# Performance work log

Hardware: AMD Instinct MI355X
Metric: run time of the kernel (lower is better)

## Reference

```python
import jax, jax.numpy as jnp
import numpy as np

B, S, D = 8, 4096, 1024


def setup_inputs() -> dict:
    key = jax.random.key(0)
    k = jax.random.split(key, 6)
    scale = 1.0 / np.sqrt(D)  # torch nn.Linear default init range
    x = jax.random.normal(k[0], (B, S, D), dtype=jnp.float32)
    mask = jnp.ones((B, S), dtype=jnp.float32)
    Wu = jax.random.uniform(k[1], (D, D), jnp.float32, -scale, scale)
    bu = jax.random.uniform(k[2], (D,), jnp.float32, -scale, scale)
    Wf = jax.random.uniform(k[3], (D, D), jnp.float32, -scale, scale)
    bf = jax.random.uniform(k[4], (D,), jnp.float32, -scale, scale)
    decay_param = jnp.zeros((1,), dtype=jnp.float32)
    return {"x": x, "mask": mask, "Wu": Wu, "bu": bu, "Wf": Wf, "bf": bf, "decay_param": decay_param}


def reference(x, mask, Wu, bu, Wf, bf, decay_param):
    # decay is a learned scalar in (0,1)
    decay = jax.nn.sigmoid(decay_param)[0]
    # Batch linear_update over all timesteps at once: (B,S,D)
    upd = jnp.einsum('bsd,ed->bse', x, Wu) + bu
    m = mask[..., None]  # (B,S,1)
    # mask-gated recurrence: mem_t = a_t * mem_{t-1} + b_t
    #   a_t = mask*decay + (1-mask),  b_t = mask*update
    a = m * decay + (1.0 - m)
    b = m * upd
    a_s = jnp.swapaxes(a, 0, 1)  # (S,B,1)
    b_s = jnp.swapaxes(b, 0, 1)  # (S,B,D)

    def step(mem, ab):
        a_t, b_t = ab
        mem = a_t * mem + b_t
        return mem, mem

    mem0 = jnp.zeros((B, D), dtype=x.dtype)
    _, mem_seq = jax.lax.scan(step, mem0, (a_s, b_s))  # (S,B,D)
    mem_seq = jnp.swapaxes(mem_seq, 0, 1)  # (B,S,D)
    # Batch linear_f over all timesteps
    out = jnp.einsum('bsd,ed->bse', mem_seq, Wf) + bf
    return out
```

## Files before the change

kernel.cpp:

```cpp
#include <hip/hip_runtime.h>
#include <hip/hip_bf16.h>
#include <math.h>

#define PB 8
#define PS 4096
#define PD 1024

typedef __attribute__((ext_vector_type(8))) short bf16x8;
typedef __attribute__((ext_vector_type(4))) float f32x4;

__device__ __forceinline__ ushort f2b(float f) {
    unsigned u = __float_as_uint(f);
    unsigned r = (u + 0x7FFFu + ((u >> 16) & 1u)) >> 16;
    return (ushort)r;
}
__device__ __forceinline__ float b2f(ushort h) {
    return __uint_as_float(((unsigned)h) << 16);
}

__device__ __forceinline__ void gl2lds16(const void* g, void* l) {
    __builtin_amdgcn_global_load_lds(
        (const __attribute__((address_space(1))) void*)g,
        (__attribute__((address_space(3))) void*)l, 16, 0, 0);
}

__global__ __launch_bounds__(256) void cvt_f32_bf16(const float* __restrict__ in,
                                                    ushort* __restrict__ out, int n) {
    int i = (blockIdx.x * 256 + threadIdx.x) * 4;
    if (i + 3 < n) {
        float4 v = *(const float4*)(in + i);
        ushort4 o;
        o.x = f2b(v.x); o.y = f2b(v.y); o.z = f2b(v.z); o.w = f2b(v.w);
        *(ushort4*)(out + i) = o;
    }
}

template <bool OUT_BF16>
__global__ __launch_bounds__(256) void gemm_bt(const ushort* __restrict__ A,
                                               const ushort* __restrict__ Bm,
                                               const float* __restrict__ bias,
                                               void* __restrict__ C,
                                               int M, int N, int K) {
    __shared__ ushort As[128 * 32];
    __shared__ ushort Bs[128 * 32];

    const int tid = threadIdx.x;
    const int lane = tid & 63;
    const int wave = tid >> 6;
    const int nbn = N >> 7;
    const int bn = blockIdx.x % nbn;
    const int bm = blockIdx.x / nbn;
    const int wm = wave >> 1, wn = wave & 1;
    const int l15 = lane & 15, quad = lane >> 4;

    const int e0 = wave * 512 + lane * 8;
    const int sr = e0 >> 5;
    const int sc = e0 & 31;
    const ushort* Ag = A + (size_t)(bm * 128 + sr) * K + sc;
    const ushort* Bg = Bm + (size_t)(bn * 128 + sr) * K + sc;
    ushort* Asw = As + wave * 512;
    ushort* Bsw = Bs + wave * 512;

    f32x4 acc[4][4];
#pragma unroll
    for (int i = 0; i < 4; ++i)
#pragma unroll
        for (int j = 0; j < 4; ++j) acc[i][j] = (f32x4){0.f, 0.f, 0.f, 0.f};

    for (int k0 = 0; k0 < K; k0 += 32) {
        __syncthreads();
        gl2lds16(Ag + k0, Asw);
        gl2lds16(Ag + k0 + (size_t)64 * K, Asw + 2048);
        gl2lds16(Bg + k0, Bsw);
        gl2lds16(Bg + k0 + (size_t)64 * K, Bsw + 2048);
        __syncthreads();

        bf16x8 af[4], bfr[4];
#pragma unroll
        for (int i = 0; i < 4; ++i)
            af[i] = *(const bf16x8*)(As + (wm * 64 + i * 16 + l15) * 32 + quad * 8);
#pragma unroll
        for (int j = 0; j < 4; ++j)
            bfr[j] = *(const bf16x8*)(Bs + (wn * 64 + j * 16 + l15) * 32 + quad * 8);
#pragma unroll
        for (int i = 0; i < 4; ++i)
#pragma unroll
            for (int j = 0; j < 4; ++j)
                acc[i][j] = __builtin_amdgcn_mfma_f32_16x16x32_bf16(af[i], bfr[j], acc[i][j], 0, 0, 0);
    }

    const int gm0 = bm * 128 + wm * 64;
    const int gn0 = bn * 128 + wn * 64;
    float bv[4];
#pragma unroll
    for (int j = 0; j < 4; ++j) bv[j] = bias[gn0 + j * 16 + l15];
#pragma unroll
    for (int i = 0; i < 4; ++i) {
#pragma unroll
        for (int j = 0; j < 4; ++j) {
            const int col = gn0 + j * 16 + l15;
#pragma unroll
            for (int r = 0; r < 4; ++r) {
                const int row = gm0 + i * 16 + quad * 4 + r;
                float v = acc[i][j][r] + bv[j];
                if (OUT_BF16)
                    ((ushort*)C)[(size_t)row * N + col] = f2b(v);
                else
                    ((float*)C)[(size_t)row * N + col] = v;
            }
        }
    }
}

__global__ __launch_bounds__(256) void scan_partial(const ushort* __restrict__ upd,
                                                    const float* __restrict__ mask,
                                                    const float* __restrict__ dp,
                                                    float* __restrict__ Bc,
                                                    float* __restrict__ Ac,
                                                    int S, int D, int C) {
    const int c = blockIdx.x % C;
    const int b = blockIdx.x / C;
    const int L = S / C;
    const int d0 = threadIdx.x * 4;
    const float decay = 1.f / (1.f + expf(-dp[0]));
    const ushort* up = upd + ((size_t)b * S + (size_t)c * L) * D + d0;
    const float* mp = mask + (size_t)b * S + (size_t)c * L;
    float aA = 1.f;
    float b0 = 0.f, b1 = 0.f, b2 = 0.f, b3 = 0.f;
    for (int s = 0; s < L; ++s) {
        float m = mp[s];
        float a = m * decay + (1.f - m);
        ushort4 u = *(const ushort4*)(up + (size_t)s * D);
        aA *= a;
        b0 = a * b0 + m * b2f(u.x);
        b1 = a * b1 + m * b2f(u.y);
        b2 = a * b2 + m * b2f(u.z);
        b3 = a * b3 + m * b2f(u.w);
    }
    *(float4*)(Bc + (size_t)blockIdx.x * D + d0) = make_float4(b0, b1, b2, b3);
    if (threadIdx.x == 0) Ac[blockIdx.x] = aA;
}

__global__ __launch_bounds__(256) void scan_prefix(const float* __restrict__ Ac,
                                                   const float* __restrict__ Bc,
                                                   float* __restrict__ Mn, int D, int C) {
    int gid = blockIdx.x * 256 + threadIdx.x;
    int b = gid / D;
    int d = gid - b * D;
    float mem = 0.f;
    for (int c = 0; c < C; ++c) {
        size_t idx = ((size_t)(b * C + c)) * D + d;
        Mn[idx] = mem;
        mem = Ac[b * C + c] * mem + Bc[idx];
    }
}

__global__ __launch_bounds__(256) void scan_final(const ushort* __restrict__ upd,
                                                  const float* __restrict__ mask,
                                                  const float* __restrict__ dp,
                                                  const float* __restrict__ Mn,
                                                  ushort* __restrict__ ms,
                                                  int S, int D, int C) {
    const int c = blockIdx.x % C;
    const int b = blockIdx.x / C;
    const int L = S / C;
    const int d0 = threadIdx.x * 4;
    const float decay = 1.f / (1.f + expf(-dp[0]));
    const ushort* up = upd + ((size_t)b * S + (size_t)c * L) * D + d0;
    ushort* op = ms + ((size_t)b * S + (size_t)c * L) * D + d0;
    const float* mp = mask + (size_t)b * S + (size_t)c * L;
    float4 m0 = *(const float4*)(Mn + (size_t)blockIdx.x * D + d0);
    float v0 = m0.x, v1 = m0.y, v2 = m0.z, v3 = m0.w;
    for (int s = 0; s < L; ++s) {
        float m = mp[s];
        float a = m * decay + (1.f - m);
        ushort4 u = *(const ushort4*)(up + (size_t)s * D);
        v0 = a * v0 + m * b2f(u.x);
        v1 = a * v1 + m * b2f(u.y);
        v2 = a * v2 + m * b2f(u.z);
        v3 = a * v3 + m * b2f(u.w);
        ushort4 o;
        o.x = f2b(v0); o.y = f2b(v1); o.z = f2b(v2); o.w = f2b(v3);
        *(ushort4*)(op + (size_t)s * D) = o;
    }
}

extern "C" void kernel_launch(void* const* d_in, const int* in_sizes, int n_in,
                              void* d_out, int out_size, void* d_ws, size_t ws_size,
                              hipStream_t stream) {
    const float* x    = (const float*)d_in[0];
    const float* mask = (const float*)d_in[1];
    const float* Wu   = (const float*)d_in[2];
    const float* bu   = (const float*)d_in[3];
    const float* Wf   = (const float*)d_in[4];
    const float* bfv  = (const float*)d_in[5];
    const float* dp   = (const float*)d_in[6];

    const int B = PB, S = PS, D = PD;
    const int M = B * S;
    const int C = 128;

    char* ws = (char*)d_ws;
    ushort* xb   = (ushort*)(ws);
    ushort* updb = (ushort*)(ws + 67108864);
    ushort* memb = (ushort*)(ws + 134217728);
    ushort* Wub  = (ushort*)(ws + 201326592);
    ushort* Wfb  = (ushort*)(ws + 203423744);
    float*  Bc   = (float*)(ws + 205520896);
    float*  Mn   = (float*)(ws + 209715200);
    float*  Ac   = (float*)(ws + 213909504);

    const int nx = B * S * D;
    cvt_f32_bf16<<<nx / 1024, 256, 0, stream>>>(x, xb, nx);
    cvt_f32_bf16<<<(D * D) / 1024, 256, 0, stream>>>(Wu, Wub, D * D);
    cvt_f32_bf16<<<(D * D) / 1024, 256, 0, stream>>>(Wf, Wfb, D * D);

    dim3 g1((M / 128) * (D / 128));
    gemm_bt<true><<<g1, 256, 0, stream>>>(xb, Wub, bu, (void*)updb, M, D, D);

    scan_partial<<<B * C, 256, 0, stream>>>(updb, mask, dp, Bc, Ac, S, D, C);
    scan_prefix<<<(B * D) / 256, 256, 0, stream>>>(Ac, Bc, Mn, D, C);
    scan_final<<<B * C, 256, 0, stream>>>(updb, mask, dp, Mn, memb, S, D, C);

    gemm_bt<false><<<g1, 256, 0, stream>>>(memb, Wfb, bfv, d_out, M, D, D);
}
```

Before: 509.5 us.

## Swizzle GEMM LDS layout, remap blocks per XCD, merge weight casts, halve scan chunks

The GEMM now XOR-swizzles the 16-byte column groups when loading global data into LDS and applies the matching swizzle when reading fragments, to cut LDS bank conflicts. Blocks are remapped so each of the 8 XCDs handles a contiguous range of M tiles, which should improve L2 reuse of the A rows. The two weight conversion kernels are merged into one launch. The scan chunk count drops from 128 to 64, giving fewer, longer chunks per batch, which changes the balance between parallelism and prefix-pass work.

Result: faster. 482.0 us (-5.4%).

```diff
diff --git a/kernel.cpp b/kernel.cpp
--- a/kernel.cpp
+++ b/kernel.cpp
@@ -35,6 +35,20 @@
     }
 }
 
+__global__ __launch_bounds__(256) void cvt_w2(const float* __restrict__ Wu,
+                                              const float* __restrict__ Wf,
+                                              ushort* __restrict__ Wub,
+                                              ushort* __restrict__ Wfb, int n) {
+    int i = (blockIdx.x * 256 + threadIdx.x) * 4;
+    const float* in = (i < n) ? Wu : Wf;
+    ushort* out = (i < n) ? Wub : Wfb;
+    int j = (i < n) ? i : i - n;
+    float4 v = *(const float4*)(in + j);
+    ushort4 o;
+    o.x = f2b(v.x); o.y = f2b(v.y); o.z = f2b(v.z); o.w = f2b(v.w);
+    *(ushort4*)(out + j) = o;
+}
+
 template <bool OUT_BF16>
 __global__ __launch_bounds__(256) void gemm_bt(const ushort* __restrict__ A,
                                                const ushort* __restrict__ Bm,
@@ -48,16 +62,17 @@
     const int lane = tid & 63;
     const int wave = tid >> 6;
     const int nbn = N >> 7;
-    const int bn = blockIdx.x % nbn;
-    const int bm = blockIdx.x / nbn;
+    const int xcd = blockIdx.x & 7;
+    const int g = blockIdx.x >> 3;
+    const int bm = xcd * ((M >> 7) >> 3) + g / nbn;
+    const int bn = g % nbn;
     const int wm = wave >> 1, wn = wave & 1;
     const int l15 = lane & 15, quad = lane >> 4;
 
-    const int e0 = wave * 512 + lane * 8;
-    const int sr = e0 >> 5;
-    const int sc = e0 & 31;
-    const ushort* Ag = A + (size_t)(bm * 128 + sr) * K + sc;
-    const ushort* Bg = Bm + (size_t)(bn * 128 + sr) * K + sc;
+    const int grow = wave * 16 + (lane >> 2);
+    const int gx = (lane & 3) ^ ((lane >> 3) & 3);
+    const ushort* Ag = A + (size_t)(bm * 128 + grow) * K + gx * 8;
+    const ushort* Bg = Bm + (size_t)(bn * 128 + grow) * K + gx * 8;
     ushort* Asw = As + wave * 512;
     ushort* Bsw = Bs + wave * 512;
 
@@ -66,6 +81,9 @@
     for (int i = 0; i < 4; ++i)
 #pragma unroll
         for (int j = 0; j < 4; ++j) acc[i][j] = (f32x4){0.f, 0.f, 0.f, 0.f};
+
+    const int rsw = (l15 >> 1) & 3;
+    const int aoff = (quad ^ rsw) * 8;
 
     for (int k0 = 0; k0 < K; k0 += 32) {
         __syncthreads();
@@ -78,10 +96,10 @@
         bf16x8 af[4], bfr[4];
 #pragma unroll
         for (int i = 0; i < 4; ++i)
-            af[i] = *(const bf16x8*)(As + (wm * 64 + i * 16 + l15) * 32 + quad * 8);
+            af[i] = *(const bf16x8*)(As + (wm * 64 + i * 16 + l15) * 32 + aoff);
 #pragma unroll
         for (int j = 0; j < 4; ++j)
-            bfr[j] = *(const bf16x8*)(Bs + (wn * 64 + j * 16 + l15) * 32 + quad * 8);
+            bfr[j] = *(const bf16x8*)(Bs + (wn * 64 + j * 16 + l15) * 32 + aoff);
 #pragma unroll
         for (int i = 0; i < 4; ++i)
 #pragma unroll
@@ -198,7 +216,7 @@
 
     const int B = PB, S = PS, D = PD;
     const int M = B * S;
-    const int C = 128;
+    const int C = 64;
 
     char* ws = (char*)d_ws;
     ushort* xb   = (ushort*)(ws);
@@ -212,8 +230,7 @@
 
     const int nx = B * S * D;
     cvt_f32_bf16<<<nx / 1024, 256, 0, stream>>>(x, xb, nx);
-    cvt_f32_bf16<<<(D * D) / 1024, 256, 0, stream>>>(Wu, Wub, D * D);
-    cvt_f32_bf16<<<(D * D) / 1024, 256, 0, stream>>>(Wf, Wfb, D * D);
+    cvt_w2<<<(2 * D * D) / 1024, 256, 0, stream>>>(Wu, Wf, Wub, Wfb, D * D);
 
     dim3 g1((M / 128) * (D / 128));
     gemm_bt<true><<<g1, 256, 0, stream>>>(xb, Wub, bu, (void*)updb, M, D, D);
```
